# Optimization experiments

Hardware: AMD Instinct MI355X
Metric: run time of the kernel (lower is better)

The kernel has to match this reference:

```python
import jax, jax.numpy as jnp
import numpy as np

B, S, N, F, G, H = 32, 512, 64, 16, 64, 256  # batch, seq, nodes, in_feat, gcn_hidden, gru_hidden
EPS = 1e-5


def setup_inputs() -> dict:
    key = jax.random.key(0)
    ks = jax.random.split(key, 24)
    def rn(k, shape, scale):
        return jax.random.normal(k, shape, dtype=jnp.float32) * scale
    inp = {
        'x': jax.random.normal(ks[0], (B, S, N, F), dtype=jnp.float32),
        'adj': jax.random.uniform(ks[1], (N, N), dtype=jnp.float32) / N,
        # GCN layer 0: input_dim -> G ; layer 1: G -> G
        'W0': rn(ks[2], (F, G), 1.0 / np.sqrt(F)),
        'b0': jnp.zeros((G,), jnp.float32),
        'W1': rn(ks[3], (G, G), 1.0 / np.sqrt(G)),
        'b1': jnp.zeros((G,), jnp.float32),
        # BatchNorm1d(num_nodes), eval mode (running stats)
        'bn_g': 1.0 + rn(ks[4], (N,), 0.1),
        'bn_b': rn(ks[5], (N,), 0.1),
        'bn_m': rn(ks[6], (N,), 0.1),
        'bn_v': 0.5 + jax.random.uniform(ks[7], (N,), dtype=jnp.float32),
        # GRU layer 0 (input N*G -> H), gate order r,z,n as in torch
        'Wih0': rn(ks[8], (3 * H, N * G), 1.0 / np.sqrt(N * G)),
        'Whh0': rn(ks[9], (3 * H, H), 1.0 / np.sqrt(H)),
        'bih0': rn(ks[10], (3 * H,), 0.02),
        'bhh0': rn(ks[11], (3 * H,), 0.02),
        # GRU layer 1 (H -> H)
        'Wih1': rn(ks[12], (3 * H, H), 1.0 / np.sqrt(H)),
        'Whh1': rn(ks[13], (3 * H, H), 1.0 / np.sqrt(H)),
        'bih1': rn(ks[14], (3 * H,), 0.02),
        'bhh1': rn(ks[15], (3 * H,), 0.02),
        # head: fc1 H -> H//2, fc2 H//2 -> N*output_dim (output_dim=1)
        'fc1_w': rn(ks[16], (H, H // 2), 1.0 / np.sqrt(H)),
        'fc1_b': jnp.zeros((H // 2,), jnp.float32),
        'fc2_w': rn(ks[17], (H // 2, N), 1.0 / np.sqrt(H // 2)),
        'fc2_b': jnp.zeros((N,), jnp.float32),
    }
    return inp


def _gru_layer(xs, Wih, Whh, bih, bhh):
    # xs: [B, S, D] -> ys: [B, S, H]; torch GRU cell math, gate order r,z,n
    b, s, _ = xs.shape
    h0 = jnp.zeros((b, Whh.shape[1]), xs.dtype)
    def step(h, x_t):
        gi = x_t @ Wih.T + bih
        gh = h @ Whh.T + bhh
        ir, iz, inn = jnp.split(gi, 3, axis=-1)
        hr, hz, hn = jnp.split(gh, 3, axis=-1)
        r = jax.nn.sigmoid(ir + hr)
        z = jax.nn.sigmoid(iz + hz)
        n = jnp.tanh(inn + r * hn)
        h_new = (1.0 - z) * n + z * h
        return h_new, h_new
    _, ys = jax.lax.scan(step, h0, jnp.swapaxes(xs, 0, 1))  # scan over time
    return jnp.swapaxes(ys, 0, 1)


def reference(x, adj, W0, b0, W1, b1, bn_g, bn_b, bn_m, bn_v,
              Wih0, Whh0, bih0, bhh0, Wih1, Whh1, bih1, bhh1,
              fc1_w, fc1_b, fc2_w, fc2_b):
    b, s, n, _ = x.shape
    g = W0.shape[1]
    # GCN layer 0 over all timesteps at once: adj @ h @ W + b, then ReLU
    h = jax.nn.relu(jnp.einsum('uv,bsvf,fg->bsug', adj, x, W0) + b0)
    # BatchNorm1d over the node channel (eval mode); dropout = identity (eval)
    inv = jax.lax.rsqrt(bn_v + EPS)
    h = (h - bn_m[:, None]) * (inv * bn_g)[:, None] + bn_b[:, None]
    # GCN layer 1 (last layer: no BN/dropout)
    h = jax.nn.relu(jnp.einsum('uv,bsvf,fg->bsug', adj, h, W1) + b1)
    # flatten nodes*features -> GRU temporal input [B, S, N*G]
    seq = h.reshape(b, s, n * g)
    y = _gru_layer(seq, Wih0, Whh0, bih0, bhh0)
    y = _gru_layer(y, Wih1, Whh1, bih1, bhh1)  # inter-layer dropout = identity (eval)
    last = y[:, -1, :]                         # [B, H]
    o = jax.nn.relu(last @ fc1_w + fc1_b)
    o = o @ fc2_w + fc2_b                      # [B, N*output_dim]
    return o.reshape(b, n, 1)
```

## Files before the change

kernel.cpp:

```cpp
#include <hip/hip_runtime.h>
#include <hip/hip_bf16.h>


#define EPS_BN 1e-5f

typedef float f32x4 __attribute__((ext_vector_type(4)));
typedef unsigned u32x4v __attribute__((ext_vector_type(4)));

#define GRU_BARRIER() do {                       \
    asm volatile("" ::: "memory");               \
    asm volatile("s_waitcnt lgkmcnt(0)");        \
    __builtin_amdgcn_s_barrier();                \
    asm volatile("" ::: "memory");               \
  } while (0)

#define MFMA_VV(c, a, b) asm volatile("v_mfma_f32_16x16x32_f16 %0, %1, %2, %0" \
                                      : "+v"(c) : "v"(a), "v"(b))
#define MFMA_A(c, a, b) asm volatile("v_mfma_f32_16x16x32_f16 %0, %1, %2, %0" \
                                     : "+v"(c) : "v"(a), "a"(b))

#define GLOAD_LDS16(gp, lp) \
  __builtin_amdgcn_global_load_lds( \
      (const __attribute__((address_space(1))) void*)(gp), \
      (__attribute__((address_space(3))) void*)(lp), 16, 0, 0)

__global__ void k_split16(const float* __restrict__ src,
                          _Float16* __restrict__ hi, _Float16* __restrict__ lo,
                          int n) {
  int i = blockIdx.x * 256 + threadIdx.x;
  if (i >= n) return;
  float v = src[i];
  _Float16 h = (_Float16)v;
  hi[i] = h;
  lo[i] = (_Float16)(v - (float)h);
}

__global__ void k_pack_frag(const float* __restrict__ whh, uint4* __restrict__ wp) {
  int tid = blockIdx.x * 256 + threadIdx.x;
  if (tid >= 24576) return;
  int l = tid & 63;
  int rest = tid >> 6;
  int ks = rest & 7; rest >>= 3;
  int nt = rest % 6;
  int w  = rest / 6;
  int n  = 16 * w + 128 * nt + (l & 15);
  int kb = ks * 32 + (l >> 4) * 8;
  const float* src = whh + (size_t)n * 256 + kb;
  unsigned dw[4];
#pragma unroll
  for (int d = 0; d < 4; ++d) {
    unsigned short lo = __builtin_bit_cast(unsigned short, (_Float16)src[2 * d]);
    unsigned short hi = __builtin_bit_cast(unsigned short, (_Float16)src[2 * d + 1]);
    dw[d] = (unsigned)lo | ((unsigned)hi << 16);
  }
  wp[tid] = make_uint4(dw[0], dw[1], dw[2], dw[3]);
}

__global__ void k_pack_gcn(const float* __restrict__ adj, const float* __restrict__ W1,
                           uint4* __restrict__ adjFh, uint4* __restrict__ adjFl,
                           uint4* __restrict__ w1Fh, uint4* __restrict__ w1Fl) {
  int tid = blockIdx.x * 256 + threadIdx.x;
  if (tid >= 1024) return;
  int l = tid & 63;
  int fi = (tid >> 6) & 7;
  bool isW1 = tid >= 512;
  int tile = fi >> 1, ks = fi & 1;
  int rc = tile * 16 + (l & 15);
  int kb = ks * 32 + (l >> 4) * 8;
  unsigned hdw[4], ldw[4];
#pragma unroll
  for (int d2 = 0; d2 < 4; ++d2) {
    unsigned short hv2[2], lv2[2];
#pragma unroll
    for (int e = 0; e < 2; ++e) {
      int k = kb + 2 * d2 + e;
      float v = isW1 ? W1[k * 64 + rc] : adj[rc * 64 + k];
      _Float16 hv = (_Float16)v;
      _Float16 lv = (_Float16)(v - (float)hv);
      hv2[e] = __builtin_bit_cast(unsigned short, hv);
      lv2[e] = __builtin_bit_cast(unsigned short, lv);
    }
    hdw[d2] = (unsigned)hv2[0] | ((unsigned)hv2[1] << 16);
    ldw[d2] = (unsigned)lv2[0] | ((unsigned)lv2[1] << 16);
  }
  uint4 hq = make_uint4(hdw[0], hdw[1], hdw[2], hdw[3]);
  uint4 lq = make_uint4(ldw[0], ldw[1], ldw[2], ldw[3]);
  if (isW1) { w1Fh[fi * 64 + l] = hq; w1Fl[fi * 64 + l] = lq; }
  else      { adjFh[fi * 64 + l] = hq; adjFl[fi * 64 + l] = lq; }
}

static __device__ __forceinline__ unsigned pk2(float a, float b, float& ra, float& rb) {
  _Float16 ha = (_Float16)a, hb = (_Float16)b;
  ra = a - (float)ha; rb = b - (float)hb;
  return (unsigned)__builtin_bit_cast(unsigned short, ha) |
         ((unsigned)__builtin_bit_cast(unsigned short, hb) << 16);
}
static __device__ __forceinline__ unsigned pk2r(float a, float b) {
  _Float16 ha = (_Float16)a, hb = (_Float16)b;
  return (unsigned)__builtin_bit_cast(unsigned short, ha) |
         ((unsigned)__builtin_bit_cast(unsigned short, hb) << 16);
}

__global__ __launch_bounds__(256) void k_gcn(
    const float* __restrict__ x,
    const float* __restrict__ adj,
    const float* __restrict__ W0, const float* __restrict__ b0,
    const uint4* __restrict__ adjFh, const uint4* __restrict__ adjFl,
    const uint4* __restrict__ w1Fh, const uint4* __restrict__ w1Fl,
    const float* __restrict__ b1,
    const float* __restrict__ bn_g, const float* __restrict__ bn_b,
    const float* __restrict__ bn_m, const float* __restrict__ bn_v,
    _Float16* __restrict__ seqh, _Float16* __restrict__ seql, int base)
{
  __shared__ float AsT[4096];
  __shared__ float Xs[1024];
  __shared__ __align__(16) _Float16 Hsh[64 * 72], Hsl[64 * 72];
  __shared__ __align__(16) _Float16 Qth[64 * 72], Qtl[64 * 72];
  __shared__ float bnm_s[64], bns_s[64], bnb_s[64];

  const int t = threadIdx.x;
  const int lane = t & 63;
  const int w = t >> 6;
  const int m = base + blockIdx.x;

  {
    const float4* a4 = (const float4*)adj;
#pragma unroll
    for (int p = 0; p < 4; ++p) {
      const int idx = t + 256 * p;
      const float4 av = a4[idx];
      const int u = idx >> 4, v4 = (idx & 15) * 4;
      AsT[(v4 + 0) * 64 + u] = av.x;
      AsT[(v4 + 1) * 64 + u] = av.y;
      AsT[(v4 + 2) * 64 + u] = av.z;
      AsT[(v4 + 3) * 64 + u] = av.w;
    }
    ((float4*)Xs)[t] = ((const float4*)(x + (size_t)m * 1024))[t];
  }
  if (t < 64) {
    bns_s[t] = rsqrtf(bn_v[t] + EPS_BN) * bn_g[t];
    bnm_s[t] = bn_m[t];
    bnb_s[t] = bn_b[t];
  }
  float w0r[16];
#pragma unroll
  for (int f = 0; f < 16; ++f) w0r[f] = W0[f * 64 + lane];
  const float b0v = b0[lane];
  __syncthreads();

  float axr[4] = {0.f, 0.f, 0.f, 0.f};
  const int f0 = w * 4;
#pragma unroll
  for (int v = 0; v < 64; ++v) {
    const float a_vu = AsT[v * 64 + lane];
    const float4 xv = *(const float4*)&Xs[v * 16 + f0];
    axr[0] = fmaf(a_vu, xv.x, axr[0]);
    axr[1] = fmaf(a_vu, xv.y, axr[1]);
    axr[2] = fmaf(a_vu, xv.z, axr[2]);
    axr[3] = fmaf(a_vu, xv.w, axr[3]);
  }
  __syncthreads();
#pragma unroll
  for (int j = 0; j < 4; ++j) Xs[lane * 16 + f0 + j] = axr[j];
  __syncthreads();

#pragma unroll
  for (int uu = 0; uu < 16; ++uu) {
    const int u = w * 16 + uu;
    float acc = 0.f;
#pragma unroll
    for (int f = 0; f < 16; ++f) acc += Xs[u * 16 + f] * w0r[f];
    float h1 = fmaxf(acc + b0v, 0.f);
    h1 = (h1 - bnm_s[u]) * bns_s[u] + bnb_s[u];
    const _Float16 hh = (_Float16)h1;
    Hsh[u * 72 + lane] = hh;
    Hsl[u * 72 + lane] = (_Float16)(h1 - (float)hh);
  }
  __syncthreads();

  {
    const int rb = (16 * w + (lane & 15)) * 72 + (lane >> 4) * 8;
    const u32x4v ah0 = *(const u32x4v*)&Hsh[rb];
    const u32x4v ah1 = *(const u32x4v*)&Hsh[rb + 32];
    const u32x4v al0 = *(const u32x4v*)&Hsl[rb];
    const u32x4v al1 = *(const u32x4v*)&Hsl[rb + 32];
    u32x4v bh[4][2], bl[4][2];
#pragma unroll
    for (int gt = 0; gt < 4; ++gt)
#pragma unroll
      for (int ks = 0; ks < 2; ++ks) {
        bh[gt][ks] = *(const u32x4v*)&w1Fh[(gt * 2 + ks) * 64 + lane];
        bl[gt][ks] = *(const u32x4v*)&w1Fl[(gt * 2 + ks) * 64 + lane];
      }
    f32x4 qa[4] = {};
#pragma unroll
    for (int gt = 0; gt < 4; ++gt) MFMA_VV(qa[gt], ah0, bh[gt][0]);
#pragma unroll
    for (int gt = 0; gt < 4; ++gt) MFMA_VV(qa[gt], ah1, bh[gt][1]);
#pragma unroll
    for (int gt = 0; gt < 4; ++gt) MFMA_VV(qa[gt], al0, bh[gt][0]);
#pragma unroll
    for (int gt = 0; gt < 4; ++gt) MFMA_VV(qa[gt], al1, bh[gt][1]);
#pragma unroll
    for (int gt = 0; gt < 4; ++gt) MFMA_VV(qa[gt], ah0, bl[gt][0]);
#pragma unroll
    for (int gt = 0; gt < 4; ++gt) MFMA_VV(qa[gt], ah1, bl[gt][1]);
    asm volatile("s_nop 7\n\ts_nop 7");
#pragma unroll
    for (int gt = 0; gt < 4; ++gt) {
      const int g = 16 * gt + (lane & 15);
      float r0, r1, r2, r3;
      uint2 uh, ul;
      uh.x = pk2(qa[gt].x, qa[gt].y, r0, r1);
      uh.y = pk2(qa[gt].z, qa[gt].w, r2, r3);
      ul.x = pk2r(r0, r1);
      ul.y = pk2r(r2, r3);
      *(uint2*)&Qth[g * 72 + 16 * w + (lane >> 4) * 4] = uh;
      *(uint2*)&Qtl[g * 72 + 16 * w + (lane >> 4) * 4] = ul;
    }
  }
  __syncthreads();

  {
    u32x4v aah[2], aal[2];
#pragma unroll
    for (int ks = 0; ks < 2; ++ks) {
      aah[ks] = *(const u32x4v*)&adjFh[(w * 2 + ks) * 64 + lane];
      aal[ks] = *(const u32x4v*)&adjFl[(w * 2 + ks) * 64 + lane];
    }
    u32x4v qbh[4][2], qbl[4][2];
#pragma unroll
    for (int gt = 0; gt < 4; ++gt)
#pragma unroll
      for (int ks = 0; ks < 2; ++ks) {
        const int rb3 = (16 * gt + (lane & 15)) * 72 + ks * 32 + (lane >> 4) * 8;
        qbh[gt][ks] = *(const u32x4v*)&Qth[rb3];
        qbl[gt][ks] = *(const u32x4v*)&Qtl[rb3];
      }
    f32x4 oa[4] = {};
#pragma unroll
    for (int gt = 0; gt < 4; ++gt) MFMA_VV(oa[gt], aah[0], qbh[gt][0]);
#pragma unroll
    for (int gt = 0; gt < 4; ++gt) MFMA_VV(oa[gt], aah[1], qbh[gt][1]);
#pragma unroll
    for (int gt = 0; gt < 4; ++gt) MFMA_VV(oa[gt], aal[0], qbh[gt][0]);
#pragma unroll
    for (int gt = 0; gt < 4; ++gt) MFMA_VV(oa[gt], aal[1], qbh[gt][1]);
#pragma unroll
    for (int gt = 0; gt < 4; ++gt) MFMA_VV(oa[gt], aah[0], qbl[gt][0]);
#pragma unroll
    for (int gt = 0; gt < 4; ++gt) MFMA_VV(oa[gt], aah[1], qbl[gt][1]);
    asm volatile("s_nop 7\n\ts_nop 7");

    _Float16* oh = seqh + (size_t)blockIdx.x * 4096;
    _Float16* ol = seql + (size_t)blockIdx.x * 4096;
    const int ub = 16 * w + (lane >> 4) * 4;
#pragma unroll
    for (int gt = 0; gt < 4; ++gt) {
      const int g = 16 * gt + (lane & 15);
      const float bv = b1[g];
#pragma unroll
      for (int q = 0; q < 4; ++q) {
        const float val = fmaxf(oa[gt][q] + bv, 0.f);
        const _Float16 hv = (_Float16)val;
        oh[(ub + q) * 64 + g] = hv;
        ol[(ub + q) * 64 + g] = (_Float16)(val - (float)hv);
      }
    }
  }
}

__global__ __launch_bounds__(256, 2) void k_gemm_lds(
    const _Float16* __restrict__ Ah, const _Float16* __restrict__ Al,
    const _Float16* __restrict__ Bh, const _Float16* __restrict__ Bl,
    const float* __restrict__ bias,
    float* __restrict__ C,
    int K, int mBlocks)
{
  __shared__ u32x4v frag[2][32][64];
  const int bid = blockIdx.x;
  const int mb = bid % mBlocks;
  const int nb = bid / mBlocks;
  const int t = threadIdx.x;
  const int w = t >> 6, l = t & 63;
  const int m0 = mb * 128, n0 = nb * 128;
  const int mh = w >> 1, nh = w & 1;
  const int row = l & 15;

  const _Float16* src[8];
#pragma unroll
  for (int s = 0; s < 8; ++s) {
    const int gs = w * 8 + s;
    const bool isB = gs >= 16;
    const int tile = (gs & 15) >> 1;
    const int hl = gs & 1;
    const _Float16* base = isB ? (hl ? Bl : Bh) : (hl ? Al : Ah);
    const int r = (isB ? n0 : m0) + 16 * tile + row;
    src[s] = base + (size_t)r * K + ((l >> 4) * 8);
  }

  f32x4 acc[4][4] = {};

#pragma unroll
  for (int s = 0; s < 8; ++s)
    GLOAD_LDS16(src[s], &frag[0][w * 8 + s][0]);
  __syncthreads();

  int cur = 0;
#pragma unroll 1
  for (int kt = 0; kt < K; kt += 32) {
    const bool more = (kt + 32) < K;
    if (more) {
#pragma unroll
      for (int s = 0; s < 8; ++s)
        GLOAD_LDS16(src[s] + kt + 32, &frag[cur ^ 1][w * 8 + s][0]);
    }

    u32x4v afh[4], afl[4], bfh[4], bfl[4];
#pragma unroll
    for (int i = 0; i < 4; ++i) {
      afh[i] = frag[cur][2 * (mh * 4 + i)][l];
      afl[i] = frag[cur][2 * (mh * 4 + i) + 1][l];
      bfh[i] = frag[cur][16 + 2 * (nh * 4 + i)][l];
      bfl[i] = frag[cur][16 + 2 * (nh * 4 + i) + 1][l];
    }

#pragma unroll
    for (int mi = 0; mi < 4; ++mi)
#pragma unroll
      for (int ni = 0; ni < 4; ++ni)
        MFMA_VV(acc[mi][ni], afh[mi], bfh[ni]);
#pragma unroll
    for (int mi = 0; mi < 4; ++mi)
#pragma unroll
      for (int ni = 0; ni < 4; ++ni)
        MFMA_VV(acc[mi][ni], afl[mi], bfh[ni]);
#pragma unroll
    for (int mi = 0; mi < 4; ++mi)
#pragma unroll
      for (int ni = 0; ni < 4; ++ni)
        MFMA_VV(acc[mi][ni], afh[mi], bfl[ni]);

    __syncthreads();
    cur ^= 1;
  }

  asm volatile("s_nop 7\n\ts_nop 7");

  const int m0w = m0 + mh * 64;
  const int n0w = n0 + nh * 64;
  const int r4 = (l >> 4) * 4;
#pragma unroll
  for (int ni = 0; ni < 4; ++ni) {
    const float bv = bias[n0w + 16 * ni + row];
#pragma unroll
    for (int mi = 0; mi < 4; ++mi) {
      float* cp = C + (size_t)(m0w + 16 * mi + r4) * 768 + n0w + 16 * ni + row;
      cp[0]    = acc[mi][ni].x + bv;
      cp[768]  = acc[mi][ni].y + bv;
      cp[1536] = acc[mi][ni].z + bv;
      cp[2304] = acc[mi][ni].w + bv;
    }
  }
}

template <bool WF16, bool LASTONLY>
__global__ __launch_bounds__(512, 2) void k_gru(
    const float* __restrict__ gi,
    const uint4* __restrict__ wp,
    const float* __restrict__ bhh,
    float* __restrict__ ys,
    _Float16* __restrict__ ysh,
    _Float16* __restrict__ ysl)
{
  const int b = blockIdx.x;
  const int t = threadIdx.x;
  const int w = t >> 6;
  const int l = t & 63;

  __shared__ __align__(16) _Float16 h2[2][256];

  const u32x4v* wp4 = (const u32x4v*)wp;
  const int wbase = w * 6;

#define LBK(nt, ks) const u32x4v b##nt##_##ks = wp4[(((wbase + nt) * 8 + ks) << 6) + l];
#define LBNT(nt) LBK(nt,0) LBK(nt,1) LBK(nt,2) LBK(nt,3) \
                 LBK(nt,4) LBK(nt,5) LBK(nt,6) LBK(nt,7)
  LBNT(0) LBNT(1) LBNT(2) LBNT(3) LBNT(4) LBNT(5)
#undef LBNT
#undef LBK

  const int half = (l >> 4) & 1;
  const int j = 16 * w + (l & 15) + 128 * half;
  const bool act = (l < 32);
  float br = 0.f, bz = 0.f, bn = 0.f;
  float hold = 0.f;
  if (act) { br = bhh[j]; bz = bhh[256 + j]; bn = bhh[512 + j]; }
  if (t < 256) { h2[0][t] = (_Float16)0.f; h2[1][t] = (_Float16)0.f; }
  __syncthreads();

  const float* gib = gi + (size_t)b * 512 * 768;
  const char* h2c = (const char*)h2;
  const int g16 = (l >> 4) * 16;
  int cur = 0;

#pragma unroll 1
  for (int step = 0; step < 512; ++step) {
    float ir = 0.f, iz = 0.f, inn = 0.f;
    if (act) {
      const float* g = gib + (size_t)step * 768;
      ir = g[j]; iz = g[256 + j]; inn = g[512 + j];
    }

    f32x4 c0 = {0.f,0.f,0.f,0.f}, c1 = c0, c2 = c0, c3 = c0, c4 = c0, c5 = c0;

#define DOT_KS(ks) { \
    const u32x4v a = *(const u32x4v*)(h2c + cur * 512 + (ks) * 64 + g16); \
    MFMA_A(c0, a, b0_##ks); MFMA_A(c1, a, b1_##ks); MFMA_A(c2, a, b2_##ks); \
    MFMA_A(c3, a, b3_##ks); MFMA_A(c4, a, b4_##ks); MFMA_A(c5, a, b5_##ks); }
    DOT_KS(0) DOT_KS(1) DOT_KS(2) DOT_KS(3)
    DOT_KS(4) DOT_KS(5) DOT_KS(6) DOT_KS(7)
#undef DOT_KS
    asm volatile("s_nop 7\n\ts_nop 7");

    if (act) {
      const float cr = half ? c1.x : c0.x;
      const float cz = half ? c3.x : c2.x;
      const float cn = half ? c5.x : c4.x;
      const float r = __builtin_amdgcn_rcpf(1.f + __expf(-(ir + cr + br)));
      const float z = __builtin_amdgcn_rcpf(1.f + __expf(-(iz + cz + bz)));
      const float e2 = __expf(2.f * (inn + r * (cn + bn)));
      const float n = 1.f - 2.f * __builtin_amdgcn_rcpf(e2 + 1.f);
      hold = (1.f - z) * n + z * hold;
      h2[cur ^ 1][j] = (_Float16)hold;
      const size_t rowi = (size_t)b * 512 + step;
      if (WF16) {
        const _Float16 hh = (_Float16)hold;
        ysh[rowi * 256 + j] = hh;
        ysl[rowi * 256 + j] = (_Float16)(hold - (float)hh);
      }
      if (LASTONLY) {
        if (step == 511) ys[rowi * 256 + j] = hold;
      }
    }
    GRU_BARRIER();
    cur ^= 1;
  }
}

__global__ __launch_bounds__(128) void k_head(
    const float* __restrict__ ys1,
    const float* __restrict__ fc1w, const float* __restrict__ fc1b,
    const float* __restrict__ fc2w, const float* __restrict__ fc2b,
    float* __restrict__ out)
{
  __shared__ float last[256];
  __shared__ float o1[128];
  const int b = blockIdx.x, t = threadIdx.x;
  const float* src = ys1 + (size_t)(b * 512 + 511) * 256;
  last[t] = src[t];
  last[128 + t] = src[128 + t];
  __syncthreads();
  float acc = fc1b[t];
#pragma unroll 8
  for (int k = 0; k < 256; ++k) acc += last[k] * fc1w[k * 128 + t];
  o1[t] = fmaxf(acc, 0.f);
  __syncthreads();
  if (t < 64) {
    float acc2 = fc2b[t];
#pragma unroll 8
    for (int i = 0; i < 128; ++i) acc2 += o1[i] * fc2w[i * 64 + t];
    out[b * 64 + t] = acc2;
  }
}

extern "C" void kernel_launch(void* const* d_in, const int* in_sizes, int n_in,
                              void* d_out, int out_size, void* d_ws, size_t ws_size,
                              hipStream_t stream)
{
  const float* x    = (const float*)d_in[0];
  const float* adj  = (const float*)d_in[1];
  const float* W0   = (const float*)d_in[2];
  const float* b0   = (const float*)d_in[3];
  const float* W1   = (const float*)d_in[4];
  const float* b1   = (const float*)d_in[5];
  const float* bng  = (const float*)d_in[6];
  const float* bnbb = (const float*)d_in[7];
  const float* bnm  = (const float*)d_in[8];
  const float* bnv  = (const float*)d_in[9];
  const float* Wih0 = (const float*)d_in[10];
  const float* Whh0 = (const float*)d_in[11];
  const float* bih0 = (const float*)d_in[12];
  const float* bhh0 = (const float*)d_in[13];
  const float* Wih1 = (const float*)d_in[14];
  const float* Whh1 = (const float*)d_in[15];
  const float* bih1 = (const float*)d_in[16];
  const float* bhh1 = (const float*)d_in[17];
  const float* fc1w = (const float*)d_in[18];
  const float* fc1b = (const float*)d_in[19];
  const float* fc2w = (const float*)d_in[20];
  const float* fc2b = (const float*)d_in[21];
  float* out = (float*)d_out;

  float* ws = (float*)d_ws;
  const size_t fixed = (size_t)16384 * 768 + (size_t)16384 * 256
                     + 2 * ((size_t)16384 * 128)
                     + 2 * 98304
                     + 2 * ((size_t)768 * 4096 / 2)
                     + 2 * ((size_t)768 * 256 / 2)
                     + 4 * 2048;
  int CHUNK = 16384;
  while (CHUNK > 128 && ((size_t)CHUNK * 4096 + fixed) * 4 > ws_size) CHUNK >>= 1;

  size_t off = 0;
  _Float16* seqh = (_Float16*)(ws + off); off += (size_t)CHUNK * 2048;
  _Float16* seql = (_Float16*)(ws + off); off += (size_t)CHUNK * 2048;
  float* gi      = ws + off; off += (size_t)16384 * 768;
  float* ys1     = ws + off; off += (size_t)16384 * 256;
  _Float16* ysh  = (_Float16*)(ws + off); off += (size_t)16384 * 128;
  _Float16* ysl  = (_Float16*)(ws + off); off += (size_t)16384 * 128;
  uint4* wp0     = (uint4*)(ws + off); off += 98304;
  uint4* wp1     = (uint4*)(ws + off); off += 98304;
  _Float16* bh0  = (_Float16*)(ws + off); off += (size_t)768 * 2048;
  _Float16* bl0  = (_Float16*)(ws + off); off += (size_t)768 * 2048;
  _Float16* bh1  = (_Float16*)(ws + off); off += (size_t)768 * 128;
  _Float16* bl1  = (_Float16*)(ws + off); off += (size_t)768 * 128;
  uint4* adjFh   = (uint4*)(ws + off); off += 2048;
  uint4* adjFl   = (uint4*)(ws + off); off += 2048;
  uint4* w1Fh    = (uint4*)(ws + off); off += 2048;
  uint4* w1Fl    = (uint4*)(ws + off); off += 2048;

  k_pack_frag<<<96, 256, 0, stream>>>(Whh0, wp0);
  k_pack_frag<<<96, 256, 0, stream>>>(Whh1, wp1);
  k_pack_gcn<<<4, 256, 0, stream>>>(adj, W1, adjFh, adjFl, w1Fh, w1Fl);
  k_split16<<<(3145728 + 255) / 256, 256, 0, stream>>>(Wih0, bh0, bl0, 3145728);
  k_split16<<<(196608 + 255) / 256, 256, 0, stream>>>(Wih1, bh1, bl1, 196608);

  const int nChunks = 16384 / CHUNK;
  for (int ci = 0; ci < nChunks; ++ci) {
    const int base = ci * CHUNK;
    k_gcn<<<CHUNK, 256, 0, stream>>>(x, adj, W0, b0, adjFh, adjFl, w1Fh, w1Fl,
                                     b1, bng, bnbb, bnm, bnv, seqh, seql, base);
    const int mB = CHUNK / 128;
    k_gemm_lds<<<mB * 6, 256, 0, stream>>>(seqh, seql, bh0, bl0, bih0,
                                           gi + (size_t)base * 768, 4096, mB);
  }
  k_gru<true, false><<<32, 512, 0, stream>>>(gi, wp0, bhh0, nullptr, ysh, ysl);
  k_gemm_lds<<<128 * 6, 256, 0, stream>>>(ysh, ysl, bh1, bl1, bih1, gi, 256, 128);
  k_gru<false, true><<<32, 512, 0, stream>>>(gi, wp1, bhh1, ys1, nullptr, nullptr);
  k_head<<<32, 128, 0, stream>>>(ys1, fc1w, fc1b, fc2w, fc2b, out);
}
```

Baseline: 2.150 ms.

## Fuse two GRU layers into one persistent kernel with flag-based pipelining

Replaces the sequential GRU layer 0, the layer-1 input GEMM and GRU layer 1 launches with a single 64-block kernel. The first 32 blocks run layer 0 and publish progress through atomic counters every 16 steps. The other 32 blocks wait for each 128-step chunk, compute that chunk's layer-1 input projection with MFMA, then run layer-1 recurrence, so both layers' serial recurrences overlap. This relies on all 64 blocks being co-resident for the spin-wait to be safe, and reuses the seq buffer as gi1 storage.

```diff
diff --git a/kernel.cpp b/kernel.cpp
--- a/kernel.cpp
+++ b/kernel.cpp
@@ -446,6 +446,166 @@
     GRU_BARRIER();
     cur ^= 1;
   }
+}
+
+__global__ __launch_bounds__(512, 2) void k_gru_fused(
+    const float* __restrict__ gi0,
+    float* __restrict__ gi1,
+    const uint4* __restrict__ wp0, const uint4* __restrict__ wp1,
+    const float* __restrict__ bhh0, const float* __restrict__ bhh1,
+    const _Float16* __restrict__ bh1, const _Float16* __restrict__ bl1,
+    const float* __restrict__ bih1,
+    float* __restrict__ ys1,
+    _Float16* __restrict__ ysh, _Float16* __restrict__ ysl,
+    int* __restrict__ prog)
+{
+  const int bid = blockIdx.x;
+  const bool role0 = bid < 32;
+  const int b = role0 ? bid : bid - 32;
+  const int t = threadIdx.x;
+  const int w = t >> 6;
+  const int l = t & 63;
+
+  __shared__ __align__(16) _Float16 h2[2][256];
+
+  const u32x4v* wp4 = (const u32x4v*)(role0 ? wp0 : wp1);
+  const float* bhh = role0 ? bhh0 : bhh1;
+  const int wbase = w * 6;
+
+#define LBK(nt, ks) const u32x4v b##nt##_##ks = wp4[(((wbase + nt) * 8 + ks) << 6) + l];
+#define LBNT(nt) LBK(nt,0) LBK(nt,1) LBK(nt,2) LBK(nt,3) \
+                 LBK(nt,4) LBK(nt,5) LBK(nt,6) LBK(nt,7)
+  LBNT(0) LBNT(1) LBNT(2) LBNT(3) LBNT(4) LBNT(5)
+#undef LBNT
+#undef LBK
+
+  const int half = (l >> 4) & 1;
+  const int j = 16 * w + (l & 15) + 128 * half;
+  const bool act = (l < 32);
+  float br = 0.f, bz = 0.f, bn = 0.f;
+  float hold = 0.f;
+  if (act) { br = bhh[j]; bz = bhh[256 + j]; bn = bhh[512 + j]; }
+  if (t < 256) { h2[0][t] = (_Float16)0.f; h2[1][t] = (_Float16)0.f; }
+  __syncthreads();
+
+  const char* h2c = (const char*)h2;
+  const int g16 = (l >> 4) * 16;
+  int cur = 0;
+
+#define STEP_BODY(gibase, step, DO_WF16, DO_LAST) { \
+    float ir = 0.f, iz = 0.f, inn = 0.f; \
+    if (act) { \
+      const float* g = (gibase) + (size_t)(step) * 768; \
+      ir = g[j]; iz = g[256 + j]; inn = g[512 + j]; \
+    } \
+    f32x4 c0 = {0.f,0.f,0.f,0.f}, c1 = c0, c2 = c0, c3 = c0, c4 = c0, c5 = c0; \
+    { const u32x4v a = *(const u32x4v*)(h2c + cur * 512 + 0 * 64 + g16); \
+      MFMA_A(c0, a, b0_0); MFMA_A(c1, a, b1_0); MFMA_A(c2, a, b2_0); \
+      MFMA_A(c3, a, b3_0); MFMA_A(c4, a, b4_0); MFMA_A(c5, a, b5_0); } \
+    { const u32x4v a = *(const u32x4v*)(h2c + cur * 512 + 1 * 64 + g16); \
+      MFMA_A(c0, a, b0_1); MFMA_A(c1, a, b1_1); MFMA_A(c2, a, b2_1); \
+      MFMA_A(c3, a, b3_1); MFMA_A(c4, a, b4_1); MFMA_A(c5, a, b5_1); } \
+    { const u32x4v a = *(const u32x4v*)(h2c + cur * 512 + 2 * 64 + g16); \
+      MFMA_A(c0, a, b0_2); MFMA_A(c1, a, b1_2); MFMA_A(c2, a, b2_2); \
+      MFMA_A(c3, a, b3_2); MFMA_A(c4, a, b4_2); MFMA_A(c5, a, b5_2); } \
+    { const u32x4v a = *(const u32x4v*)(h2c + cur * 512 + 3 * 64 + g16); \
+      MFMA_A(c0, a, b0_3); MFMA_A(c1, a, b1_3); MFMA_A(c2, a, b2_3); \
+      MFMA_A(c3, a, b3_3); MFMA_A(c4, a, b4_3); MFMA_A(c5, a, b5_3); } \
+    { const u32x4v a = *(const u32x4v*)(h2c + cur * 512 + 4 * 64 + g16); \
+      MFMA_A(c0, a, b0_4); MFMA_A(c1, a, b1_4); MFMA_A(c2, a, b2_4); \
+      MFMA_A(c3, a, b3_4); MFMA_A(c4, a, b4_4); MFMA_A(c5, a, b5_4); } \
+    { const u32x4v a = *(const u32x4v*)(h2c + cur * 512 + 5 * 64 + g16); \
+      MFMA_A(c0, a, b0_5); MFMA_A(c1, a, b1_5); MFMA_A(c2, a, b2_5); \
+      MFMA_A(c3, a, b3_5); MFMA_A(c4, a, b4_5); MFMA_A(c5, a, b5_5); } \
+    { const u32x4v a = *(const u32x4v*)(h2c + cur * 512 + 6 * 64 + g16); \
+      MFMA_A(c0, a, b0_6); MFMA_A(c1, a, b1_6); MFMA_A(c2, a, b2_6); \
+      MFMA_A(c3, a, b3_6); MFMA_A(c4, a, b4_6); MFMA_A(c5, a, b5_6); } \
+    { const u32x4v a = *(const u32x4v*)(h2c + cur * 512 + 7 * 64 + g16); \
+      MFMA_A(c0, a, b0_7); MFMA_A(c1, a, b1_7); MFMA_A(c2, a, b2_7); \
+      MFMA_A(c3, a, b3_7); MFMA_A(c4, a, b4_7); MFMA_A(c5, a, b5_7); } \
+    asm volatile("s_nop 7\n\ts_nop 7"); \
+    if (act) { \
+      const float cr = half ? c1.x : c0.x; \
+      const float cz = half ? c3.x : c2.x; \
+      const float cn = half ? c5.x : c4.x; \
+      const float r = __builtin_amdgcn_rcpf(1.f + __expf(-(ir + cr + br))); \
+      const float z = __builtin_amdgcn_rcpf(1.f + __expf(-(iz + cz + bz))); \
+      const float e2 = __expf(2.f * (inn + r * (cn + bn))); \
+      const float n = 1.f - 2.f * __builtin_amdgcn_rcpf(e2 + 1.f); \
+      hold = (1.f - z) * n + z * hold; \
+      h2[cur ^ 1][j] = (_Float16)hold; \
+      const size_t rowi = (size_t)b * 512 + (step); \
+      if (DO_WF16) { \
+        const _Float16 hh = (_Float16)hold; \
+        ysh[rowi * 256 + j] = hh; \
+        ysl[rowi * 256 + j] = (_Float16)(hold - (float)hh); \
+      } \
+      if (DO_LAST) { if ((step) == 511) ys1[rowi * 256 + j] = hold; } \
+    } \
+  }
+
+  if (role0) {
+    const float* gib = gi0 + (size_t)b * 512 * 768;
+#pragma unroll 1
+    for (int step = 0; step < 512; ++step) {
+      STEP_BODY(gib, step, true, false)
+      if ((step & 15) == 15) {
+        __syncthreads();
+        if (t == 0)
+          __hip_atomic_store(&prog[b], step + 1, __ATOMIC_RELEASE,
+                             __HIP_MEMORY_SCOPE_AGENT);
+      } else {
+        GRU_BARRIER();
+      }
+      cur ^= 1;
+    }
+  } else {
+    float* gi1b = gi1 + (size_t)b * 512 * 768;
+#pragma unroll 1
+    for (int g = 0; g < 4; ++g) {
+      if (t == 0) {
+        while (__hip_atomic_load(&prog[b], __ATOMIC_ACQUIRE,
+                                 __HIP_MEMORY_SCOPE_AGENT) < 128 * (g + 1))
+          __builtin_amdgcn_s_sleep(8);
+      }
+      __syncthreads();
+      {
+        const size_t arow =
+            ((size_t)b * 512 + 128 * g + 16 * w + (l & 15)) * 256 + (l >> 4) * 8;
+        const size_t orowb = (size_t)128 * g + 16 * w + 4 * (l >> 4);
+#pragma unroll 1
+        for (int ct = 0; ct < 48; ++ct) {
+          const int col = 16 * ct + (l & 15);
+          const size_t brow = (size_t)col * 256 + (l >> 4) * 8;
+          f32x4 acc = {0.f, 0.f, 0.f, 0.f};
+#pragma unroll
+          for (int ks = 0; ks < 8; ++ks) {
+            const u32x4v a_h = *(const u32x4v*)(ysh + arow + 32 * ks);
+            const u32x4v a_l = *(const u32x4v*)(ysl + arow + 32 * ks);
+            const u32x4v bfh = *(const u32x4v*)(bh1 + brow + 32 * ks);
+            const u32x4v bfl = *(const u32x4v*)(bl1 + brow + 32 * ks);
+            MFMA_VV(acc, a_h, bfh);
+            MFMA_VV(acc, a_l, bfh);
+            MFMA_VV(acc, a_h, bfl);
+          }
+          asm volatile("s_nop 7\n\ts_nop 7");
+          const float bv = bih1[col];
+#pragma unroll
+          for (int q = 0; q < 4; ++q)
+            gi1b[(orowb + q) * 768 + col] = acc[q] + bv;
+        }
+      }
+      __syncthreads();
+#pragma unroll 1
+      for (int s2 = 0; s2 < 128; ++s2) {
+        const int step = 128 * g + s2;
+        STEP_BODY(gi1b, step, false, true)
+        GRU_BARRIER();
+        cur ^= 1;
+      }
+    }
+  }
+#undef STEP_BODY
 }
 
 __global__ __launch_bounds__(128) void k_head(
@@ -508,7 +668,7 @@
                      + 2 * 98304
                      + 2 * ((size_t)768 * 4096 / 2)
                      + 2 * ((size_t)768 * 256 / 2)
-                     + 4 * 2048;
+                     + 4 * 2048 + 64;
   int CHUNK = 16384;
   while (CHUNK > 128 && ((size_t)CHUNK * 4096 + fixed) * 4 > ws_size) CHUNK >>= 1;
 
@@ -529,6 +689,8 @@
   uint4* adjFl   = (uint4*)(ws + off); off += 2048;
   uint4* w1Fh    = (uint4*)(ws + off); off += 2048;
   uint4* w1Fl    = (uint4*)(ws + off); off += 2048;
+  int*   prog    = (int*)(ws + off);  off += 64;
+  float* gi1     = (float*)seqh;
 
   k_pack_frag<<<96, 256, 0, stream>>>(Whh0, wp0);
   k_pack_frag<<<96, 256, 0, stream>>>(Whh1, wp1);
@@ -545,8 +707,15 @@
     k_gemm_lds<<<mB * 6, 256, 0, stream>>>(seqh, seql, bh0, bl0, bih0,
                                            gi + (size_t)base * 768, 4096, mB);
   }
-  k_gru<true, false><<<32, 512, 0, stream>>>(gi, wp0, bhh0, nullptr, ysh, ysl);
-  k_gemm_lds<<<128 * 6, 256, 0, stream>>>(ysh, ysl, bh1, bl1, bih1, gi, 256, 128);
-  k_gru<false, true><<<32, 512, 0, stream>>>(gi, wp1, bhh1, ys1, nullptr, nullptr);
+
+  if (CHUNK >= 4096) {
+    hipMemsetAsync(prog, 0, 32 * sizeof(int), stream);
+    k_gru_fused<<<64, 512, 0, stream>>>(gi, gi1, wp0, wp1, bhh0, bhh1,
+                                        bh1, bl1, bih1, ys1, ysh, ysl, prog);
+  } else {
+    k_gru<true, false><<<32, 512, 0, stream>>>(gi, wp0, bhh0, nullptr, ysh, ysl);
+    k_gemm_lds<<<128 * 6, 256, 0, stream>>>(ysh, ysl, bh1, bl1, bih1, gi, 256, 128);
+    k_gru<false, true><<<32, 512, 0, stream>>>(gi, wp1, bhh1, ys1, nullptr, nullptr);
+  }
   k_head<<<32, 128, 0, stream>>>(ys1, fc1w, fc1b, fc2w, fc2b, out);
 }
```

New measurement: 3.115 ms. 1.45x slower.
